# Kernel tuning notes

Hardware: AMD Instinct MI355X
Metric: run time of the kernel (lower is better)

The kernel has to match this reference:

```python
import jax, jax.numpy as jnp
import numpy as np

B_, C_, H_, W_, N_ = 2, 256, 64, 64, 16


def setup_inputs() -> dict:
    key = jax.random.key(0)
    ks = jax.random.split(key, 6)
    return {
        "features": jax.random.normal(ks[0], (B_, C_, H_, W_), jnp.float32),
        "A_log": jax.random.normal(ks[1], (C_, N_), jnp.float32) * 0.5,
        "D": jax.random.normal(ks[2], (C_,), jnp.float32),
        "W_delta": jax.random.normal(ks[3], (C_, C_), jnp.float32) * 0.02,
        "b_delta": jnp.zeros((C_,), jnp.float32),
        "W_B": jax.random.normal(ks[4], (C_, N_), jnp.float32) * 0.02,
        "W_C": jax.random.normal(ks[5], (C_, N_), jnp.float32) * 0.02,
    }


def _selective_scan(x, A_log, D, W_delta, b_delta, W_B, W_C):
    # x: (B, L, C) -> (B, L, C). Canonical S6 selective scan (mamba corrector).
    delta = jax.nn.softplus(x @ W_delta + b_delta)          # (B, L, C)
    Bm = x @ W_B                                            # (B, L, N)
    Cm = x @ W_C                                            # (B, L, N)
    A = -jnp.exp(A_log)                                     # (C, N), negative real
    dA = jnp.exp(delta[..., None] * A)                      # (B, L, C, N)
    dBx = (delta * x)[..., None] * Bm[:, :, None, :]        # (B, L, C, N)

    def combine(left, right):
        a_l, b_l = left
        a_r, b_r = right
        return (a_l * a_r, a_r * b_l + b_r)

    # h_t = dA_t * h_{t-1} + dBx_t, computed in parallel over L
    _, h = jax.lax.associative_scan(combine, (dA, dBx), axis=1)
    y = jnp.einsum('blcn,bln->blc', h, Cm) + x * D          # (B, L, C)
    return y


def reference(features, A_log, D, W_delta, b_delta, W_B, W_C):
    B, C, H, W = features.shape
    corr = lambda x: _selective_scan(x, A_log, D, W_delta, b_delta, W_B, W_C)

    # direction 1: row-major forward
    flat = features.reshape(B, C, H * W).transpose(0, 2, 1)        # (B, HW, C)
    out1 = corr(flat)
    # direction 2: row-major reversed
    out2 = jnp.flip(corr(jnp.flip(flat, axis=1)), axis=1)
    # direction 3: rows flipped vertically (flip over H), scan, flip back
    rows = features.transpose(0, 2, 3, 1)                          # (B, H, W, C)
    rows_f = jnp.flip(rows, axis=1).reshape(B, H * W, C)
    out3 = jnp.flip(corr(rows_f).reshape(B, H, W, C), axis=1).reshape(B, H * W, C)
    # direction 4: column-major, flipped over W, scan, flip + transpose back
    cols = features.transpose(0, 3, 2, 1)                          # (B, W, H, C)
    cols_f = jnp.flip(cols, axis=1).reshape(B, W * H, C)
    out4 = jnp.flip(corr(cols_f).reshape(B, W, H, C), axis=1)
    out4 = out4.transpose(0, 2, 1, 3).reshape(B, H * W, C)

    mamba_out = (out1 + out2 + out3 + out4) / 4                    # (B, HW, C)
    return mamba_out.transpose(0, 2, 1).reshape(B, C, H, W)
```

## Files before the change

kernel.cpp:

```cpp
#include <hip/hip_runtime.h>
#include <cstdint>
#include <cstddef>

#define BB 2
#define CC 256
#define NN 16
#define LL 4096
#define NCH 128
#define CLEN 32
#define LOG2E 1.4426950408889634f

__device__ __forceinline__ float softplus_f(float z) {
    return fmaxf(z, 0.f) + log1pf(expf(-fabsf(z)));
}

__global__ __launch_bounds__(256) void k1_delta_gemm(
    const float* __restrict__ feat, const float* __restrict__ Wd,
    const float* __restrict__ bd, const float* __restrict__ WB,
    const float* __restrict__ WC, float* __restrict__ du,
    float* __restrict__ Bm, float* __restrict__ Cm)
{
    int ctile = blockIdx.x & 3;
    int lt    = (blockIdx.x >> 2) & 63;
    int b     = blockIdx.x >> 8;
    int l0 = lt * 64, c0 = ctile * 64;
    __shared__ float As[16][64];
    __shared__ float Bs[16][64];
    __shared__ float sW[8192];
    int tx = threadIdx.x & 15, ty = threadIdx.x >> 4;
    int arow = ty;
    int acol = tx * 4;
    float acc[4][4] = {};
    const bool doBC = (ctile == 0);
    int lloc = threadIdx.x & 63;
    int half = threadIdx.x >> 6;
    int nb   = (half & 1) * 8;
    float accBC[8] = {};
    if (doBC) {
        for (int i = threadIdx.x; i < 4096; i += 256) {
            sW[i]        = WB[i];
            sW[4096 + i] = WC[i];
        }
    }
    const float* fbase = feat + (size_t)b * CC * LL;
    for (int k0 = 0; k0 < 256; k0 += 16) {
        __syncthreads();
        *(float4*)&As[arow][acol] = *(const float4*)&fbase[(size_t)(k0 + arow) * LL + l0 + acol];
        *(float4*)&Bs[arow][acol] = *(const float4*)&Wd[(size_t)(k0 + arow) * CC + c0 + acol];
        __syncthreads();
        #pragma unroll
        for (int kk = 0; kk < 16; ++kk) {
            float4 a = *(float4*)&As[kk][ty * 4];
            float4 w = *(float4*)&Bs[kk][tx * 4];
            float av[4] = {a.x, a.y, a.z, a.w};
            float wv[4] = {w.x, w.y, w.z, w.w};
            #pragma unroll
            for (int i = 0; i < 4; ++i)
                #pragma unroll
                for (int j = 0; j < 4; ++j)
                    acc[i][j] = fmaf(av[i], wv[j], acc[i][j]);
        }
        if (doBC) {
            const float* wbase = &sW[(half >> 1) * 4096 + nb];
            #pragma unroll
            for (int kk = 0; kk < 16; ++kk) {
                float xv = As[kk][lloc];
                float4 w0 = *(const float4*)&wbase[(k0 + kk) * 16];
                float4 w1 = *(const float4*)&wbase[(k0 + kk) * 16 + 4];
                accBC[0] = fmaf(xv, w0.x, accBC[0]);
                accBC[1] = fmaf(xv, w0.y, accBC[1]);
                accBC[2] = fmaf(xv, w0.z, accBC[2]);
                accBC[3] = fmaf(xv, w0.w, accBC[3]);
                accBC[4] = fmaf(xv, w1.x, accBC[4]);
                accBC[5] = fmaf(xv, w1.y, accBC[5]);
                accBC[6] = fmaf(xv, w1.z, accBC[6]);
                accBC[7] = fmaf(xv, w1.w, accBC[7]);
            }
        }
    }
    if (doBC) {
        float* dst = ((half >> 1) ? Cm : Bm) + ((size_t)b * LL + l0 + lloc) * NN + nb;
        *(float4*)&dst[0] = make_float4(accBC[0], accBC[1], accBC[2], accBC[3]);
        *(float4*)&dst[4] = make_float4(accBC[4], accBC[5], accBC[6], accBC[7]);
    }
    float bdv[4];
    #pragma unroll
    for (int j = 0; j < 4; ++j) bdv[j] = bd[c0 + tx * 4 + j];
    float4 fcol[4];
    #pragma unroll
    for (int j = 0; j < 4; ++j)
        fcol[j] = *(const float4*)&fbase[(size_t)(c0 + tx * 4 + j) * LL + l0 + ty * 4];
    float fc[4][4];
    fc[0][0]=fcol[0].x; fc[0][1]=fcol[1].x; fc[0][2]=fcol[2].x; fc[0][3]=fcol[3].x;
    fc[1][0]=fcol[0].y; fc[1][1]=fcol[1].y; fc[1][2]=fcol[2].y; fc[1][3]=fcol[3].y;
    fc[2][0]=fcol[0].z; fc[2][1]=fcol[1].z; fc[2][2]=fcol[2].z; fc[2][3]=fcol[3].z;
    fc[3][0]=fcol[0].w; fc[3][1]=fcol[1].w; fc[3][2]=fcol[2].w; fc[3][3]=fcol[3].w;
    float4* du4 = (float4*)du;
    #pragma unroll
    for (int i = 0; i < 4; ++i) {
        int l = l0 + ty * 4 + i;
        float dv[4], uv[4];
        #pragma unroll
        for (int j = 0; j < 4; ++j) {
            float z = acc[i][j] + bdv[j];
            dv[j] = softplus_f(z);
            uv[j] = dv[j] * fc[i][j];
        }
        size_t o = (((size_t)b * LL + l) * CC + c0 + tx * 4) >> 1;
        du4[o]     = make_float4(dv[0], uv[0], dv[1], uv[1]);
        du4[o + 1] = make_float4(dv[2], uv[2], dv[3], uv[3]);
    }
}

__global__ __launch_bounds__(256, 4) void p1_aggr(
    const float2* __restrict__ du, const float* __restrict__ Bm,
    const float* __restrict__ A_log, float* __restrict__ P, float* __restrict__ S)
{
    int blk = blockIdx.x;
    int cls = blk >> 8;
    int b   = (blk >> 7) & 1;
    int ch  = blk & 127;
    int p0, inner;
    if (cls == 0)      { p0 = 32 * ch;        inner = 1; }
    else if (cls == 1) { p0 = 4095 - 32 * ch; inner = -1; }
    else               { p0 = 63 - (ch >> 1) + 2048 * (ch & 1); inner = 64; }
    int c = threadIdx.x;
    __shared__ float sBm[CLEN * NN];
    for (int i = threadIdx.x; i < CLEN * NN; i += 256) {
        int j = i >> 4, n = i & 15;
        sBm[i] = Bm[((size_t)b * LL + (p0 + inner * j)) * NN + n];
    }
    float A2[NN];
    {
        const float4* al = (const float4*)(A_log + c * NN);
        #pragma unroll
        for (int q = 0; q < 4; ++q) {
            float4 v = al[q];
            A2[q*4+0] = -expf(v.x) * LOG2E;
            A2[q*4+1] = -expf(v.y) * LOG2E;
            A2[q*4+2] = -expf(v.z) * LOG2E;
            A2[q*4+3] = -expf(v.w) * LOG2E;
        }
    }
    __syncthreads();
    float Sv[NN] = {};
    float sumd = 0.f;
    const float2* dub = du + (size_t)b * LL * CC + c;
    for (int j = 0; j < CLEN; ++j) {
        float2 dv = dub[(size_t)(p0 + inner * j) * CC];
        sumd += dv.x;
        float dA[NN];
        #pragma unroll
        for (int n = 0; n < NN; ++n) dA[n] = __builtin_amdgcn_exp2f(A2[n] * dv.x);
        #pragma unroll
        for (int n = 0; n < NN; ++n)
            Sv[n] = fmaf(dA[n], Sv[n], dv.y * sBm[j * 16 + n]);
    }
    size_t base = ((size_t)((cls * 2 + b) * 128 + ch)) * 4096 + (size_t)c * 16;
    #pragma unroll
    for (int n = 0; n < NN; ++n) {
        P[base + n] = __builtin_amdgcn_exp2f(A2[n] * sumd);
        S[base + n] = Sv[n];
    }
}

__global__ __launch_bounds__(128) void p2_scan(
    const float* __restrict__ P, const float* __restrict__ S, float* __restrict__ Hin)
{
    int r = blockIdx.x * 128 + threadIdx.x;
    int cn = r & 4095;
    int db = r >> 12;
    int d = db >> 1;
    int cls = (d == 1) ? 1 : ((d == 3) ? 2 : 0);
    int b = db & 1;
    const size_t cbase = ((size_t)(cls * 2 + b) * 128) * 4096 + cn;
    const size_t obase = ((size_t)db * 128) * 4096 + cn;
    float h = 0.f;
    for (int g = 0; g < 16; ++g) {
        float pv[8], sv[8];
        #pragma unroll
        for (int i = 0; i < 8; ++i) {
            int ch = g * 8 + i;
            int chm = (d == 2) ? (126 - 2 * (ch >> 1) + (ch & 1)) : ch;
            size_t ix = cbase + (size_t)chm * 4096;
            pv[i] = P[ix];
            sv[i] = S[ix];
        }
        #pragma unroll
        for (int i = 0; i < 8; ++i) {
            Hin[obase + (size_t)(g * 8 + i) * 4096] = h;
            h = fmaf(pv[i], h, sv[i]);
        }
    }
}

__global__ __launch_bounds__(256, 4) void p3_replay(
    const float2* __restrict__ du, const float* __restrict__ Bm,
    const float* __restrict__ Cm, const float* __restrict__ A_log,
    const float* __restrict__ Hin, float* __restrict__ yA,
    float* __restrict__ yB, float* __restrict__ yC)
{
    int blk = blockIdx.x;
    int sec = blk >> 8;
    int b   = (blk >> 7) & 1;
    int ch  = blk & 127;
    int p0, inner;
    if (sec == 0)      { p0 = 32 * ch;        inner = 1; }
    else if (sec == 1) { p0 = 4095 - 32 * ch; inner = -1; }
    else               { p0 = 63 - (ch >> 1) + 2048 * (ch & 1); inner = 64; }
    int c = threadIdx.x;
    __shared__ float sBm[CLEN * NN];
    __shared__ float sCm[CLEN * NN];
    for (int i = threadIdx.x; i < CLEN * NN; i += 256) {
        int j = i >> 4, n = i & 15;
        size_t o = ((size_t)b * LL + (p0 + inner * j)) * NN + n;
        sBm[i] = Bm[o];
        sCm[i] = Cm[o];
    }
    float A2[NN];
    {
        const float4* al = (const float4*)(A_log + c * NN);
        #pragma unroll
        for (int q = 0; q < 4; ++q) {
            float4 v = al[q];
            A2[q*4+0] = -expf(v.x) * LOG2E;
            A2[q*4+1] = -expf(v.y) * LOG2E;
            A2[q*4+2] = -expf(v.z) * LOG2E;
            A2[q*4+3] = -expf(v.w) * LOG2E;
        }
    }
    const float2* dub = du + (size_t)b * LL * CC + c;

    if (sec == 0) {
        int ch2 = 126 - (ch & ~1) + (ch & 1);
        float h0[NN], h2[NN];
        {
            const float4* hp0 = (const float4*)(Hin + ((size_t)(0 * 2 + b) * 128 + ch)  * 4096 + (size_t)c * 16);
            const float4* hp2 = (const float4*)(Hin + ((size_t)(2 * 2 + b) * 128 + ch2) * 4096 + (size_t)c * 16);
            #pragma unroll
            for (int q = 0; q < 4; ++q) {
                float4 v0 = hp0[q], v2 = hp2[q];
                h0[q*4+0]=v0.x; h0[q*4+1]=v0.y; h0[q*4+2]=v0.z; h0[q*4+3]=v0.w;
                h2[q*4+0]=v2.x; h2[q*4+1]=v2.y; h2[q*4+2]=v2.z; h2[q*4+3]=v2.w;
            }
        }
        __syncthreads();
        for (int j = 0; j < CLEN; ++j) {
            int p = p0 + j;
            float2 dv = dub[(size_t)p * CC];
            float dA[NN];
            #pragma unroll
            for (int n = 0; n < NN; ++n) dA[n] = __builtin_amdgcn_exp2f(A2[n] * dv.x);
            float y0v = 0.f, y2v = 0.f;
            #pragma unroll
            for (int n = 0; n < NN; ++n) {
                float Bu = dv.y * sBm[j * 16 + n];
                float cm = sCm[j * 16 + n];
                h0[n] = fmaf(dA[n], h0[n], Bu);
                h2[n] = fmaf(dA[n], h2[n], Bu);
                y0v = fmaf(h0[n], cm, y0v);
                y2v = fmaf(h2[n], cm, y2v);
            }
            yA[((size_t)b * LL + p) * CC + c] = 0.25f * (y0v + y2v);
        }
    } else {
        int d = (sec == 1) ? 1 : 3;
        float h[NN];
        {
            const float4* hp = (const float4*)(Hin + ((size_t)(d * 2 + b) * 128 + ch) * 4096 + (size_t)c * 16);
            #pragma unroll
            for (int q = 0; q < 4; ++q) {
                float4 v = hp[q];
                h[q*4+0]=v.x; h[q*4+1]=v.y; h[q*4+2]=v.z; h[q*4+3]=v.w;
            }
        }
        __syncthreads();
        float* yD = (sec == 1) ? yB : yC;
        for (int j = 0; j < CLEN; ++j) {
            int p = p0 + inner * j;
            float2 dv = dub[(size_t)p * CC];
            float dA[NN];
            #pragma unroll
            for (int n = 0; n < NN; ++n) dA[n] = __builtin_amdgcn_exp2f(A2[n] * dv.x);
            float yv = 0.f;
            #pragma unroll
            for (int n = 0; n < NN; ++n) {
                float Bu = dv.y * sBm[j * 16 + n];
                h[n] = fmaf(dA[n], h[n], Bu);
                yv = fmaf(h[n], sCm[j * 16 + n], yv);
            }
            yD[((size_t)b * LL + p) * CC + c] = 0.25f * yv;
        }
    }
}

__global__ __launch_bounds__(256) void k6_reduce(
    const float* __restrict__ feat, const float* __restrict__ D,
    const float* __restrict__ yA, const float* __restrict__ yB,
    const float* __restrict__ yC, float* __restrict__ out)
{
    int pt = blockIdx.x & 63;
    int ct = (blockIdx.x >> 6) & 3;
    int b  = blockIdx.x >> 8;
    int p0 = pt * 64, c0 = ct * 64;
    __shared__ float tile[64 * 65];
    {
        int cl = threadIdx.x & 63;
        int pg = threadIdx.x >> 6;
        #pragma unroll
        for (int pp = 0; pp < 16; ++pp) {
            int pl = pp * 4 + pg;
            size_t ix = ((size_t)b * LL + p0 + pl) * CC + c0 + cl;
            tile[cl * 65 + pl] = yA[ix] + yB[ix] + yC[ix];
        }
    }
    __syncthreads();
    {
        int pl = threadIdx.x & 63;
        int cg = threadIdx.x >> 6;
        #pragma unroll
        for (int cc = 0; cc < 16; ++cc) {
            int cloc = cc * 4 + cg;
            int c = c0 + cloc;
            size_t o = ((size_t)b * CC + c) * LL + p0 + pl;
            out[o] = tile[cloc * 65 + pl] + feat[o] * D[c];
        }
    }
}

extern "C" void kernel_launch(void* const* d_in, const int* in_sizes, int n_in,
                              void* d_out, int out_size, void* d_ws, size_t ws_size,
                              hipStream_t stream)
{
    const float* feat  = (const float*)d_in[0];
    const float* A_log = (const float*)d_in[1];
    const float* D     = (const float*)d_in[2];
    const float* Wd    = (const float*)d_in[3];
    const float* bd    = (const float*)d_in[4];
    const float* WB    = (const float*)d_in[5];
    const float* WC    = (const float*)d_in[6];
    float* out = (float*)d_out;

    float* ws  = (float*)d_ws;
    float* du  = ws;
    float* Bm  = du  + (size_t)4194304;
    float* Cm  = Bm  + (size_t)131072;
    float* P   = Cm  + (size_t)131072;
    float* S   = P   + (size_t)3145728;
    float* Hin = S   + (size_t)3145728;
    float* yA  = Hin + (size_t)4194304;
    float* yB  = yA  + (size_t)2097152;
    float* yC  = yB  + (size_t)2097152;

    k1_delta_gemm<<<512, 256, 0, stream>>>(feat, Wd, bd, WB, WC, du, Bm, Cm);
    p1_aggr<<<768, 256, 0, stream>>>((const float2*)du, Bm, A_log, P, S);
    p2_scan<<<256, 128, 0, stream>>>(P, S, Hin);
    p3_replay<<<768, 256, 0, stream>>>((const float2*)du, Bm, Cm, A_log, Hin, yA, yB, yC);
    k6_reduce<<<512, 256, 0, stream>>>(feat, D, yA, yB, yC, out);
}
```

Baseline: 176.6 us.

## Double-buffer k1 GEMM with 64x128 tiles and read B/C weights from global

Reworks the delta GEMM kernel to use 64x128 output tiles with a 32-deep K step and register-prefetched double-buffered shared memory, halving the grid to 256 blocks. The WB/WC weights are no longer staged into a 32KB shared array and are instead read directly through wave-uniform global loads. The goal is more FMA work per shared load, one barrier per K step instead of two, and lower shared memory use. In exchange each thread holds more registers, fewer blocks are launched on a chip with many CUs, and the B/C projection now depends on cache hits for weight reads.

New measurement: 192.0 us. 1.09x slower.

```diff
diff --git a/kernel.cpp b/kernel.cpp
--- a/kernel.cpp
+++ b/kernel.cpp
@@ -8,6 +8,7 @@
 #define LL 4096
 #define NCH 128
 #define CLEN 32
+#define BKK 32
 #define LOG2E 1.4426950408889634f
 
 __device__ __forceinline__ float softplus_f(float z) {
@@ -20,53 +21,76 @@
     const float* __restrict__ WC, float* __restrict__ du,
     float* __restrict__ Bm, float* __restrict__ Cm)
 {
-    int ctile = blockIdx.x & 3;
-    int lt    = (blockIdx.x >> 2) & 63;
-    int b     = blockIdx.x >> 8;
-    int l0 = lt * 64, c0 = ctile * 64;
-    __shared__ float As[16][64];
-    __shared__ float Bs[16][64];
-    __shared__ float sW[8192];
-    int tx = threadIdx.x & 15, ty = threadIdx.x >> 4;
-    int arow = ty;
-    int acol = tx * 4;
-    float acc[4][4] = {};
-    const bool doBC = (ctile == 0);
+    int ct = blockIdx.x & 1;
+    int lt = (blockIdx.x >> 1) & 63;
+    int b  = blockIdx.x >> 7;
+    int l0 = lt * 64, c0 = ct * 128;
+    __shared__ float As[2][BKK][64];
+    __shared__ float Bs[2][BKK][128];
+    int tx = threadIdx.x & 15;
+    int ty = threadIdx.x >> 4;
+
+    const float* fbase = feat + (size_t)b * CC * LL;
+    const bool doBC = (ct == 0);
+    int halfu = __builtin_amdgcn_readfirstlane(threadIdx.x >> 6);
+    const float* wsel = (halfu >> 1) ? WC : WB;
+    int nbu = (halfu & 1) * 8;
     int lloc = threadIdx.x & 63;
-    int half = threadIdx.x >> 6;
-    int nb   = (half & 1) * 8;
+
+    int qa0 = threadIdx.x,        ra0 = qa0 >> 4, ca0 = (qa0 & 15) * 4;
+    int qa1 = threadIdx.x + 256,  ra1 = qa1 >> 4, ca1 = (qa1 & 15) * 4;
+    int rb[4], cb[4];
+    #pragma unroll
+    for (int i = 0; i < 4; ++i) {
+        int q = threadIdx.x + 256 * i;
+        rb[i] = q >> 5; cb[i] = (q & 31) * 4;
+    }
+
+    float4 pa0, pa1, pb[4];
+    pa0 = *(const float4*)&fbase[(size_t)ra0 * LL + l0 + ca0];
+    pa1 = *(const float4*)&fbase[(size_t)ra1 * LL + l0 + ca1];
+    #pragma unroll
+    for (int i = 0; i < 4; ++i)
+        pb[i] = *(const float4*)&Wd[(size_t)rb[i] * CC + c0 + cb[i]];
+    *(float4*)&As[0][ra0][ca0] = pa0;
+    *(float4*)&As[0][ra1][ca1] = pa1;
+    #pragma unroll
+    for (int i = 0; i < 4; ++i)
+        *(float4*)&Bs[0][rb[i]][cb[i]] = pb[i];
+
+    float acc[4][8] = {};
     float accBC[8] = {};
-    if (doBC) {
-        for (int i = threadIdx.x; i < 4096; i += 256) {
-            sW[i]        = WB[i];
-            sW[4096 + i] = WC[i];
-        }
-    }
-    const float* fbase = feat + (size_t)b * CC * LL;
-    for (int k0 = 0; k0 < 256; k0 += 16) {
+    int buf = 0;
+    for (int s = 0; s < 8; ++s) {
+        if (s < 7) {
+            int k0 = (s + 1) * BKK;
+            pa0 = *(const float4*)&fbase[(size_t)(k0 + ra0) * LL + l0 + ca0];
+            pa1 = *(const float4*)&fbase[(size_t)(k0 + ra1) * LL + l0 + ca1];
+            #pragma unroll
+            for (int i = 0; i < 4; ++i)
+                pb[i] = *(const float4*)&Wd[(size_t)(k0 + rb[i]) * CC + c0 + cb[i]];
+        }
         __syncthreads();
-        *(float4*)&As[arow][acol] = *(const float4*)&fbase[(size_t)(k0 + arow) * LL + l0 + acol];
-        *(float4*)&Bs[arow][acol] = *(const float4*)&Wd[(size_t)(k0 + arow) * CC + c0 + acol];
-        __syncthreads();
-        #pragma unroll
-        for (int kk = 0; kk < 16; ++kk) {
-            float4 a = *(float4*)&As[kk][ty * 4];
-            float4 w = *(float4*)&Bs[kk][tx * 4];
+        #pragma unroll
+        for (int kk = 0; kk < BKK; ++kk) {
+            float4 a  = *(float4*)&As[buf][kk][ty * 4];
+            float4 b0 = *(float4*)&Bs[buf][kk][tx * 4];
+            float4 b1 = *(float4*)&Bs[buf][kk][64 + tx * 4];
             float av[4] = {a.x, a.y, a.z, a.w};
-            float wv[4] = {w.x, w.y, w.z, w.w};
+            float bv[8] = {b0.x, b0.y, b0.z, b0.w, b1.x, b1.y, b1.z, b1.w};
             #pragma unroll
             for (int i = 0; i < 4; ++i)
                 #pragma unroll
-                for (int j = 0; j < 4; ++j)
-                    acc[i][j] = fmaf(av[i], wv[j], acc[i][j]);
+                for (int j = 0; j < 8; ++j)
+                    acc[i][j] = fmaf(av[i], bv[j], acc[i][j]);
         }
         if (doBC) {
-            const float* wbase = &sW[(half >> 1) * 4096 + nb];
-            #pragma unroll
-            for (int kk = 0; kk < 16; ++kk) {
-                float xv = As[kk][lloc];
-                float4 w0 = *(const float4*)&wbase[(k0 + kk) * 16];
-                float4 w1 = *(const float4*)&wbase[(k0 + kk) * 16 + 4];
+            int kb = s * BKK;
+            #pragma unroll
+            for (int kk = 0; kk < BKK; ++kk) {
+                float xv = As[buf][kk][lloc];
+                float4 w0 = *(const float4*)&wsel[(kb + kk) * 16 + nbu];
+                float4 w1 = *(const float4*)&wsel[(kb + kk) * 16 + nbu + 4];
                 accBC[0] = fmaf(xv, w0.x, accBC[0]);
                 accBC[1] = fmaf(xv, w0.y, accBC[1]);
                 accBC[2] = fmaf(xv, w0.z, accBC[2]);
@@ -77,38 +101,53 @@
                 accBC[7] = fmaf(xv, w1.w, accBC[7]);
             }
         }
-    }
+        if (s < 7) {
+            *(float4*)&As[buf ^ 1][ra0][ca0] = pa0;
+            *(float4*)&As[buf ^ 1][ra1][ca1] = pa1;
+            #pragma unroll
+            for (int i = 0; i < 4; ++i)
+                *(float4*)&Bs[buf ^ 1][rb[i]][cb[i]] = pb[i];
+        }
+        buf ^= 1;
+    }
+
     if (doBC) {
-        float* dst = ((half >> 1) ? Cm : Bm) + ((size_t)b * LL + l0 + lloc) * NN + nb;
+        float* dst = ((halfu >> 1) ? Cm : Bm) + ((size_t)b * LL + l0 + lloc) * NN + nbu;
         *(float4*)&dst[0] = make_float4(accBC[0], accBC[1], accBC[2], accBC[3]);
         *(float4*)&dst[4] = make_float4(accBC[4], accBC[5], accBC[6], accBC[7]);
     }
-    float bdv[4];
-    #pragma unroll
-    for (int j = 0; j < 4; ++j) bdv[j] = bd[c0 + tx * 4 + j];
-    float4 fcol[4];
-    #pragma unroll
-    for (int j = 0; j < 4; ++j)
-        fcol[j] = *(const float4*)&fbase[(size_t)(c0 + tx * 4 + j) * LL + l0 + ty * 4];
-    float fc[4][4];
-    fc[0][0]=fcol[0].x; fc[0][1]=fcol[1].x; fc[0][2]=fcol[2].x; fc[0][3]=fcol[3].x;
-    fc[1][0]=fcol[0].y; fc[1][1]=fcol[1].y; fc[1][2]=fcol[2].y; fc[1][3]=fcol[3].y;
-    fc[2][0]=fcol[0].z; fc[2][1]=fcol[1].z; fc[2][2]=fcol[2].z; fc[2][3]=fcol[3].z;
-    fc[3][0]=fcol[0].w; fc[3][1]=fcol[1].w; fc[3][2]=fcol[2].w; fc[3][3]=fcol[3].w;
+
+    float bdv[8];
+    #pragma unroll
+    for (int g = 0; g < 2; ++g)
+        #pragma unroll
+        for (int j = 0; j < 4; ++j) bdv[g * 4 + j] = bd[c0 + g * 64 + tx * 4 + j];
+    float fc[4][8];
+    #pragma unroll
+    for (int g = 0; g < 2; ++g)
+        #pragma unroll
+        for (int j = 0; j < 4; ++j) {
+            float4 v = *(const float4*)&fbase[(size_t)(c0 + g * 64 + tx * 4 + j) * LL + l0 + ty * 4];
+            fc[0][g * 4 + j] = v.x; fc[1][g * 4 + j] = v.y;
+            fc[2][g * 4 + j] = v.z; fc[3][g * 4 + j] = v.w;
+        }
     float4* du4 = (float4*)du;
     #pragma unroll
     for (int i = 0; i < 4; ++i) {
         int l = l0 + ty * 4 + i;
-        float dv[4], uv[4];
-        #pragma unroll
-        for (int j = 0; j < 4; ++j) {
-            float z = acc[i][j] + bdv[j];
-            dv[j] = softplus_f(z);
-            uv[j] = dv[j] * fc[i][j];
-        }
-        size_t o = (((size_t)b * LL + l) * CC + c0 + tx * 4) >> 1;
-        du4[o]     = make_float4(dv[0], uv[0], dv[1], uv[1]);
-        du4[o + 1] = make_float4(dv[2], uv[2], dv[3], uv[3]);
+        #pragma unroll
+        for (int g = 0; g < 2; ++g) {
+            float dv[4], uv[4];
+            #pragma unroll
+            for (int j = 0; j < 4; ++j) {
+                float z = acc[i][g * 4 + j] + bdv[g * 4 + j];
+                dv[j] = softplus_f(z);
+                uv[j] = dv[j] * fc[i][g * 4 + j];
+            }
+            size_t o = (((size_t)b * LL + l) * CC + c0 + g * 64 + tx * 4) >> 1;
+            du4[o]     = make_float4(dv[0], uv[0], dv[1], uv[1]);
+            du4[o + 1] = make_float4(dv[2], uv[2], dv[3], uv[3]);
+        }
     }
 }
 
@@ -352,7 +391,7 @@
     float* yB  = yA  + (size_t)2097152;
     float* yC  = yB  + (size_t)2097152;
 
-    k1_delta_gemm<<<512, 256, 0, stream>>>(feat, Wd, bd, WB, WC, du, Bm, Cm);
+    k1_delta_gemm<<<256, 256, 0, stream>>>(feat, Wd, bd, WB, WC, du, Bm, Cm);
     p1_aggr<<<768, 256, 0, stream>>>((const float2*)du, Bm, A_log, P, S);
     p2_scan<<<256, 128, 0, stream>>>(P, S, Hin);
     p3_replay<<<768, 256, 0, stream>>>((const float2*)du, Bm, Cm, A_log, Hin, yA, yB, yC);
```
